# Optimization experiments

Measured on AMD Instinct MI355X. Metric: run time of the kernel, lower is better.

## Reference

```python
import jax, jax.numpy as jnp
import numpy as np

NB, CODES, D = 4, 1024, 64          # n_codebooks, codes_per_book, embedding_dim
B, T, H, W = 4, 8, 32, 32
COST = 0.25                          # commitment_cost


def setup_inputs() -> dict:
    key = jax.random.key(0)
    k1, k2 = jax.random.split(key)
    z = jax.random.normal(k1, (B, NB * D, T, H, W), dtype=jnp.float32)
    embeddings = jax.random.normal(k2, (NB, CODES, D), dtype=jnp.float32)
    return {"z": z, "embeddings": embeddings}


def reference(z, embeddings):
    # (B,C,T,H,W) -> (B,T,H,W,C) -> (NB, N, D) with N = B*T*H*W
    zc = jnp.moveaxis(z, 1, -1)
    flat = zc.reshape(-1, NB, D).transpose(1, 0, 2)  # (NB, N, D)
    N = flat.shape[1]

    x2 = jnp.sum(flat * flat, axis=2, keepdims=True)                 # (NB,N,1)
    e2 = jnp.sum(embeddings * embeddings, axis=2)[:, None, :]        # (NB,1,C)
    dist = x2 - 2.0 * jnp.einsum('knd,kcd->knc', flat, embeddings) + e2
    idx = jnp.argmin(dist, axis=2)                                   # (NB, N)

    # per-book embedding gather, equivalent to torch.stack([emb[i][idx[i]]], dim=-2)
    q = jax.vmap(lambda i, e: e[i])(idx, embeddings)                 # (NB, N, D)
    quantized = q.transpose(1, 0, 2).reshape(B, T, H, W, NB * D)
    quantized = jnp.moveaxis(quantized, -1, 1)                       # (B,C,T,H,W)

    encodings = jnp.moveaxis(idx.reshape(NB, B, T, H, W), 0, -1)     # (B,T,H,W,NB)

    commitment_loss = COST * jnp.mean((z - jax.lax.stop_gradient(quantized)) ** 2)
    quantized_st = z + jax.lax.stop_gradient(quantized - z)          # straight-through

    # perplexity from code usage histogram (avoids materializing one-hot)
    counts = jax.vmap(lambda i: jnp.zeros(CODES, flat.dtype).at[i].add(1.0))(idx)
    avg_probs = counts / N
    perplexity = jnp.mean(jnp.exp(-jnp.sum(avg_probs * jnp.log(avg_probs + 1e-10), axis=1)))

    return quantized_st, encodings, commitment_loss, perplexity
```

## Files before the change

kernel.cpp:

```cpp
#include <hip/hip_runtime.h>

#define NBOOKS 4
#define CODES  1024
#define DIM    64
#define NPOS   32768
#define CCH    256
#define ENC_OFF  8388608
#define LOSS_OFF 8519680
#define PERP_OFF 8519681

#define WS_E2      0
#define WS_EHI     16384
#define WS_ELO     540672
#define WS_IDX     1064960
#define WS_CNT     1589248
#define WS_PART    1605632
#define WS_FLAGCNT 1607680
#define WS_FLAGS   1607696

typedef _Float16 f16x8 __attribute__((ext_vector_type(8)));
typedef _Float16 f16x4 __attribute__((ext_vector_type(4)));
typedef float    f32x4 __attribute__((ext_vector_type(4)));

__global__ void k_eprep2(const float* __restrict__ emb, float* __restrict__ e2,
                         _Float16* __restrict__ ehi, _Float16* __restrict__ elo,
                         int* __restrict__ counts, int* __restrict__ flagcnt) {
    int i = blockIdx.x * 256 + threadIdx.x;
    counts[i] = 0;
    if (i == 0) *flagcnt = 0;
    const float4* e = (const float4*)(emb + ((size_t)i << 6));
    _Float16* hp = ehi + ((size_t)i << 6);
    _Float16* lp = elo + ((size_t)i << 6);
    float s = 0.f;
#pragma unroll
    for (int j = 0; j < 16; ++j) {
        float4 v = e[j];
        s += v.x * v.x + v.y * v.y + v.z * v.z + v.w * v.w;
        f16x4 hv, lv;
        float m;
        m = -2.f * v.x; hv[0] = (_Float16)m; lv[0] = (_Float16)(m - (float)hv[0]);
        m = -2.f * v.y; hv[1] = (_Float16)m; lv[1] = (_Float16)(m - (float)hv[1]);
        m = -2.f * v.z; hv[2] = (_Float16)m; lv[2] = (_Float16)(m - (float)hv[2]);
        m = -2.f * v.w; hv[3] = (_Float16)m; lv[3] = (_Float16)(m - (float)hv[3]);
        *(f16x4*)&hp[j * 4] = hv;
        *(f16x4*)&lp[j * 4] = lv;
    }
    e2[i] = s;
}

__global__ void __launch_bounds__(256, 4) k_argmin_mfma(
        const float* __restrict__ z, const float* __restrict__ e2g,
        const _Float16* __restrict__ ehi, const _Float16* __restrict__ elo,
        int* __restrict__ idxbuf, int* __restrict__ flagcnt,
        int* __restrict__ flaglist) {
    __shared__ __attribute__((aligned(16))) char sE[3][8192];

    int tid = threadIdx.x;
    int wave = tid >> 6, lane = tid & 63;
    int lrow = lane >> 4, lcol = lane & 15;
    int k = blockIdx.y;
    int posbase = blockIdx.x * 128;
    int b = posbase >> 13, s0 = posbase & 8191;
    int wb = wave * 32;

    const float* zb = z + (((size_t)(b * CCH + k * DIM)) << 13) + s0 + wb;
    f16x8 Xh[2][2], Xl[2][2];
#pragma unroll
    for (int pt = 0; pt < 2; ++pt)
#pragma unroll
        for (int kc = 0; kc < 2; ++kc) {
            f16x8 hv, lv;
#pragma unroll
            for (int e = 0; e < 8; ++e) {
                int d = kc * 32 + lrow * 8 + e;
                float f = zb[((size_t)d << 13) + pt * 16 + lcol];
                _Float16 h = (_Float16)f;
                hv[e] = h;
                lv[e] = (_Float16)(f - (float)h);
            }
            Xh[pt][kc] = hv; Xl[pt][kc] = lv;
        }

    int half = tid >> 7;
    int u = tid & 127;
    int r = u >> 2, q = u & 3;
    const char* bookh = (const char*)((half ? elo : ehi) + ((size_t)k << 16));
    const char* src0 = bookh + r * 128 + q * 32;
    int c0 = 2 * q, c1 = 2 * q + 1;
    int w0 = half * 4096 + r * 128 + ((c0 ^ (r & 7)) << 4);
    int w1 = half * 4096 + r * 128 + ((c1 ^ (r & 7)) << 4);

    const float* e2p = e2g + (k << 10) + lrow * 4;

    {
        f16x8 v0 = *(const f16x8*)(src0);
        f16x8 v1 = *(const f16x8*)(src0 + 16);
        *(f16x8*)&sE[0][w0] = v0;
        *(f16x8*)&sE[0][w1] = v1;
    }
    f32x4 ce2a = *(const f32x4*)(e2p);
    f32x4 ce2b = *(const f32x4*)(e2p + 16);

    float m1f[2][4], m2f[2][4];
#pragma unroll
    for (int pt = 0; pt < 2; ++pt)
#pragma unroll
        for (int rr = 0; rr < 4; ++rr) { m1f[pt][rr] = 3.4e38f; m2f[pt][rr] = 3.4e38f; }

    int sx = (lcol & 7) << 4;
    int o0 = (lrow << 4) ^ sx;
    int o1 = ((4 + lrow) << 4) ^ sx;
    int rbase = lcol << 7;

    int cur = 0, nxt = 1, fre = 2;
    for (int it = 0; it < 32; ++it) {
        __syncthreads();
        const char* sc = sE[cur];

        const char* rb0 = sc + rbase;
        const char* rb1 = sc + 2048 + rbase;
        f16x8 eh0a = *(const f16x8*)(rb0 + o0);
        f16x8 eh1a = *(const f16x8*)(rb0 + o1);
        f16x8 el0a = *(const f16x8*)(rb0 + 4096 + o0);
        f16x8 el1a = *(const f16x8*)(rb0 + 4096 + o1);
        f16x8 eh0b = *(const f16x8*)(rb1 + o0);
        f16x8 eh1b = *(const f16x8*)(rb1 + o1);
        f16x8 el0b = *(const f16x8*)(rb1 + 4096 + o0);
        f16x8 el1b = *(const f16x8*)(rb1 + 4096 + o1);

        f16x8 nv0, nv1;
        f32x4 ne2a, ne2b;
        bool has = it < 31;
        if (has) {
            const char* sp = src0 + (size_t)(it + 1) * 4096;
            nv0 = *(const f16x8*)(sp);
            nv1 = *(const f16x8*)(sp + 16);
            ne2a = *(const f32x4*)(e2p + (it + 1) * 32);
            ne2b = *(const f32x4*)(e2p + (it + 1) * 32 + 16);
        }

#pragma unroll
        for (int st = 0; st < 2; ++st) {
            f16x8 eh0 = st ? eh0b : eh0a;
            f16x8 eh1 = st ? eh1b : eh1a;
            f16x8 el0 = st ? el0b : el0a;
            f16x8 el1 = st ? el1b : el1a;
            f32x4 e2v = st ? ce2b : ce2a;
            unsigned kit = (unsigned)(it * 2 + st);
#pragma unroll
            for (int pt = 0; pt < 2; ++pt) {
                f32x4 acc = e2v;
                acc = __builtin_amdgcn_mfma_f32_16x16x32_f16(eh0, Xh[pt][0], acc, 0, 0, 0);
                acc = __builtin_amdgcn_mfma_f32_16x16x32_f16(eh0, Xl[pt][0], acc, 0, 0, 0);
                acc = __builtin_amdgcn_mfma_f32_16x16x32_f16(el0, Xh[pt][0], acc, 0, 0, 0);
                acc = __builtin_amdgcn_mfma_f32_16x16x32_f16(eh1, Xh[pt][1], acc, 0, 0, 0);
                acc = __builtin_amdgcn_mfma_f32_16x16x32_f16(eh1, Xl[pt][1], acc, 0, 0, 0);
                acc = __builtin_amdgcn_mfma_f32_16x16x32_f16(el1, Xh[pt][1], acc, 0, 0, 0);
#pragma unroll
                for (int rr = 0; rr < 4; ++rr) {
                    float key = __uint_as_float(
                        (__float_as_uint(acc[rr]) & 0xFFFFFFC0u) | kit);
                    m2f[pt][rr] = __builtin_amdgcn_fmed3f(m1f[pt][rr], m2f[pt][rr], key);
                    m1f[pt][rr] = fminf(m1f[pt][rr], key);
                }
            }
        }

        if (has) {
            *(f16x8*)&sE[nxt][w0] = nv0;
            *(f16x8*)&sE[nxt][w1] = nv1;
            ce2a = ne2a; ce2b = ne2b;
        }
        int t = cur; cur = nxt; nxt = fre; fre = t;
    }

    float F1[2], F2[2]; int I1[2];
#pragma unroll
    for (int pt = 0; pt < 2; ++pt) {
        float f1 = 3.4e38f, f2 = 3.4e38f; int i1 = 0;
#pragma unroll
        for (int rr = 0; rr < 4; ++rr) {
            unsigned mb = __float_as_uint(m1f[pt][rr]);
            float f = __uint_as_float(mb & 0xFFFFFFC0u);
            int   c = (int)(mb & 63u) * 16 + lrow * 4 + rr;
            float g = __uint_as_float(__float_as_uint(m2f[pt][rr]) & 0xFFFFFFC0u);
            bool take = (f < f1) || (f == f1 && c < i1);
            float loser = take ? f1 : f;
            f2 = fminf(fminf(f2, g), loser);
            if (take) { f1 = f; i1 = c; }
        }
        F1[pt] = f1; F2[pt] = f2; I1[pt] = i1;
    }

#pragma unroll
    for (int off = 16; off < 64; off <<= 1) {
#pragma unroll
        for (int pt = 0; pt < 2; ++pt) {
            float om1 = __shfl_xor(F1[pt], off);
            float om2 = __shfl_xor(F2[pt], off);
            int   oi  = __shfl_xor(I1[pt], off);
            bool take = (om1 < F1[pt]) || (om1 == F1[pt] && oi < I1[pt]);
            float loser = take ? F1[pt] : om1;
            F2[pt] = fminf(fminf(F2[pt], om2), loser);
            if (take) { F1[pt] = om1; I1[pt] = oi; }
        }
    }

    if (lane < 16) {
#pragma unroll
        for (int pt = 0; pt < 2; ++pt) {
            int n = posbase + wb + pt * 16 + lane;
            idxbuf[(k << 15) + n] = I1[pt];
            float thr = fmaf(fabsf(F1[pt]), 3.2e-5f, 2.0e-3f);
            if (F2[pt] - F1[pt] < thr) {
                int slot = atomicAdd(flagcnt, 1);
                flaglist[slot] = (k << 15) + n;
            }
        }
    }
}

__global__ void __launch_bounds__(256) k_rescore(
        const float* __restrict__ z, const float* __restrict__ emb,
        const float* __restrict__ e2g, const int* __restrict__ flagcnt,
        const int* __restrict__ flaglist, int* __restrict__ idxbuf) {
    __shared__ __attribute__((aligned(16))) float xsh[64];
    __shared__ float wbest[4];
    __shared__ int   wbi[4];
    int tid = threadIdx.x;
    int wave = tid >> 6, lane = tid & 63;
    int nf = *flagcnt;
    for (int e = blockIdx.x; e < nf; e += gridDim.x) {
        int gp = flaglist[e];
        int kk = gp >> 15, n = gp & 32767;
        int bb = n >> 13, s = n & 8191;
        __syncthreads();
        if (tid < 64)
            xsh[tid] = z[(((size_t)(bb * CCH + kk * DIM + tid)) << 13) + s];
        __syncthreads();

        const f32x4* ek4 = (const f32x4*)(emb + ((size_t)kk << 16));
        const float* ee  = e2g + (kk << 10);
        const f32x4* xr4 = (const f32x4*)xsh;
        float best = 3.4e38f; int bi = 0;
#pragma unroll
        for (int cc = 0; cc < 4; ++cc) {
            int c = cc * 256 + tid;
            const f32x4* ev = ek4 + (size_t)c * 16;
            float a0 = 0.f, a1 = 0.f, a2 = 0.f, a3 = 0.f;
#pragma unroll
            for (int j = 0; j < 16; ++j) {
                f32x4 xv = xr4[j];
                f32x4 qv = ev[j];
                a0 = fmaf(xv[0], qv[0], a0); a1 = fmaf(xv[1], qv[1], a1);
                a2 = fmaf(xv[2], qv[2], a2); a3 = fmaf(xv[3], qv[3], a3);
            }
            float dist = fmaf(-2.f, (a0 + a1) + (a2 + a3), ee[c]);
            if (dist < best) { best = dist; bi = c; }
        }
#pragma unroll
        for (int off = 1; off < 64; off <<= 1) {
            float ob = __shfl_xor(best, off);
            int   oi = __shfl_xor(bi, off);
            if (ob < best || (ob == best && oi < bi)) { best = ob; bi = oi; }
        }
        if (lane == 0) { wbest[wave] = best; wbi[wave] = bi; }
        __syncthreads();
        if (tid == 0) {
            float b0 = wbest[0]; int i0 = wbi[0];
#pragma unroll
            for (int w = 1; w < 4; ++w) {
                float bw = wbest[w]; int iw = wbi[w];
                if (bw < b0 || (bw == b0 && iw < i0)) { b0 = bw; i0 = iw; }
            }
            idxbuf[gp] = i0;
        }
    }
}

__global__ void __launch_bounds__(256) k_quant(
        const float* __restrict__ z, const float* __restrict__ emb,
        const int* __restrict__ idxbuf, float* __restrict__ out,
        int* __restrict__ counts, float* __restrict__ partial) {
    int tid = threadIdx.x;
    int q = blockIdx.x * 256 + tid;
    int n0 = q * 4;
    int k = blockIdx.y;
    int b = n0 >> 13;
    int s = n0 & 8191;

    int4 bi = *(const int4*)&idxbuf[(k << 15) + n0];
    const f32x4* e0 = (const f32x4*)(emb + ((size_t)k << 16) + ((size_t)bi.x << 6));
    const f32x4* e1 = (const f32x4*)(emb + ((size_t)k << 16) + ((size_t)bi.y << 6));
    const f32x4* e2 = (const f32x4*)(emb + ((size_t)k << 16) + ((size_t)bi.z << 6));
    const f32x4* e3 = (const f32x4*)(emb + ((size_t)k << 16) + ((size_t)bi.w << 6));
    size_t base = (((size_t)(b * CCH + k * DIM)) << 13) + s;

    float sq = 0.f;
#pragma unroll
    for (int j = 0; j < 16; ++j) {
        f32x4 q0 = e0[j], q1 = e1[j], q2 = e2[j], q3 = e3[j];
#pragma unroll
        for (int i = 0; i < 4; ++i) {
            int d = j * 4 + i;
            f32x4 zv = *(const f32x4*)(z + base + ((size_t)d << 13));
            f32x4 ov = {q0[i], q1[i], q2[i], q3[i]};
            *(f32x4*)(out + base + ((size_t)d << 13)) = ov;
            f32x4 df = zv - ov;
            sq = fmaf(df[0], df[0], sq);
            sq = fmaf(df[1], df[1], sq);
            sq = fmaf(df[2], df[2], sq);
            sq = fmaf(df[3], df[3], sq);
        }
    }

    out[ENC_OFF + (size_t)(n0 + 0) * NBOOKS + k] = (float)bi.x;
    out[ENC_OFF + (size_t)(n0 + 1) * NBOOKS + k] = (float)bi.y;
    out[ENC_OFF + (size_t)(n0 + 2) * NBOOKS + k] = (float)bi.z;
    out[ENC_OFF + (size_t)(n0 + 3) * NBOOKS + k] = (float)bi.w;
    atomicAdd(&counts[(k << 10) + bi.x], 1);
    atomicAdd(&counts[(k << 10) + bi.y], 1);
    atomicAdd(&counts[(k << 10) + bi.z], 1);
    atomicAdd(&counts[(k << 10) + bi.w], 1);

    for (int off = 32; off; off >>= 1) sq += __shfl_down(sq, off, 64);
    __shared__ float red[4];
    if ((tid & 63) == 0) red[tid >> 6] = sq;
    __syncthreads();
    if (tid == 0)
        partial[blockIdx.y * gridDim.x + blockIdx.x] = (red[0] + red[1]) + (red[2] + red[3]);
}

__global__ void __launch_bounds__(256) k_fin(
        const int* __restrict__ counts, const float* __restrict__ partial,
        float* __restrict__ out) {
    __shared__ float shl[4];
    __shared__ float shp[4];
    int tid = threadIdx.x;
    int wave = tid >> 6, lane = tid & 63;

    float s = tid < 128 ? partial[tid] : 0.f;
    for (int off = 32; off; off >>= 1) s += __shfl_down(s, off, 64);
    if (lane == 0) shl[wave] = s;

    float h = 0.f;
    const int* ck = counts + (wave << 10) + lane * 16;
#pragma unroll
    for (int j = 0; j < 16; ++j) {
        float p = (float)ck[j] * (1.f / 32768.f);
        h += p * logf(p + 1e-10f);
    }
    for (int off = 32; off; off >>= 1) h += __shfl_down(h, off, 64);
    if (lane == 0) shp[wave] = expf(-h);
    __syncthreads();
    if (tid == 0) {
        out[LOSS_OFF] = 0.25f * ((shl[0] + shl[1]) + (shl[2] + shl[3])) / 8388608.f;
        out[PERP_OFF] = 0.25f * ((shp[0] + shp[1]) + (shp[2] + shp[3]));
    }
}

extern "C" void kernel_launch(void* const* d_in, const int* in_sizes, int n_in,
                              void* d_out, int out_size, void* d_ws, size_t ws_size,
                              hipStream_t stream) {
    const float* z   = (const float*)d_in[0];
    const float* emb = (const float*)d_in[1];
    float* out = (float*)d_out;
    char* ws = (char*)d_ws;

    float*    e2       = (float*)(ws + WS_E2);
    _Float16* ehi      = (_Float16*)(ws + WS_EHI);
    _Float16* elo      = (_Float16*)(ws + WS_ELO);
    int*      idxbuf   = (int*)(ws + WS_IDX);
    int*      counts   = (int*)(ws + WS_CNT);
    float*    partial  = (float*)(ws + WS_PART);
    int*      flagcnt  = (int*)(ws + WS_FLAGCNT);
    int*      flaglist = (int*)(ws + WS_FLAGS);

    k_eprep2<<<16, 256, 0, stream>>>(emb, e2, ehi, elo, counts, flagcnt);

    dim3 agrid(NPOS / 128, NBOOKS);
    k_argmin_mfma<<<agrid, 256, 0, stream>>>(z, e2, ehi, elo, idxbuf, flagcnt, flaglist);
    k_rescore<<<1024, 256, 0, stream>>>(z, emb, e2, flagcnt, flaglist, idxbuf);

    dim3 qgrid(NPOS / 1024, NBOOKS);
    k_quant<<<qgrid, 256, 0, stream>>>(z, emb, idxbuf, out, counts, partial);
    k_fin<<<1, 256, 0, stream>>>(counts, partial, out);
}
```

Baseline: 113.9 us.

## Split codebook across waves and drop LDS staging in argmin kernel

Instead of each wave taking 32 positions and streaming all 1024 codes through triple-buffered shared memory, each wave now keeps all 128 positions of the block in registers and scans its own 256-code slice, loading codebook fragments straight from global memory with register prefetch. Per-wave results go through shared memory in a cross-wave reduction that keeps best and second-best distances. This removes the per-iteration barriers and LDS traffic, and each codebook fragment is reused across 8 position tiles. In exchange register use grows a lot (occupancy hint drops from 4 to 2), there is more global/L2 traffic for the codebook, and the near-tie threshold for flagging rescoring is tightened, which changes how many points get rescored.

```diff
diff --git a/kernel.cpp b/kernel.cpp
--- a/kernel.cpp
+++ b/kernel.cpp
@@ -48,12 +48,14 @@
     e2[i] = s;
 }
 
-__global__ void __launch_bounds__(256, 4) k_argmin_mfma(
+__global__ void __launch_bounds__(256, 2) k_argmin_mfma(
         const float* __restrict__ z, const float* __restrict__ e2g,
         const _Float16* __restrict__ ehi, const _Float16* __restrict__ elo,
         int* __restrict__ idxbuf, int* __restrict__ flagcnt,
         int* __restrict__ flaglist) {
-    __shared__ __attribute__((aligned(16))) char sE[3][8192];
+    __shared__ float sF1[512];
+    __shared__ float sF2[512];
+    __shared__ int   sI1[512];
 
     int tid = threadIdx.x;
     int wave = tid >> 6, lane = tid & 63;
@@ -61,161 +63,133 @@
     int k = blockIdx.y;
     int posbase = blockIdx.x * 128;
     int b = posbase >> 13, s0 = posbase & 8191;
-    int wb = wave * 32;
-
-    const float* zb = z + (((size_t)(b * CCH + k * DIM)) << 13) + s0 + wb;
-    f16x8 Xh[2][2], Xl[2][2];
-#pragma unroll
-    for (int pt = 0; pt < 2; ++pt)
+
+    const float* zb = z + (((size_t)(b * CCH + k * DIM)) << 13) + s0;
+    f16x8 Xh[8][2], Xl[8][2];
+#pragma unroll
+    for (int bt = 0; bt < 8; ++bt)
 #pragma unroll
         for (int kc = 0; kc < 2; ++kc) {
             f16x8 hv, lv;
 #pragma unroll
             for (int e = 0; e < 8; ++e) {
                 int d = kc * 32 + lrow * 8 + e;
-                float f = zb[((size_t)d << 13) + pt * 16 + lcol];
+                float f = zb[((size_t)d << 13) + bt * 16 + lcol];
                 _Float16 h = (_Float16)f;
                 hv[e] = h;
                 lv[e] = (_Float16)(f - (float)h);
             }
-            Xh[pt][kc] = hv; Xl[pt][kc] = lv;
-        }
-
-    int half = tid >> 7;
-    int u = tid & 127;
-    int r = u >> 2, q = u & 3;
-    const char* bookh = (const char*)((half ? elo : ehi) + ((size_t)k << 16));
-    const char* src0 = bookh + r * 128 + q * 32;
-    int c0 = 2 * q, c1 = 2 * q + 1;
-    int w0 = half * 4096 + r * 128 + ((c0 ^ (r & 7)) << 4);
-    int w1 = half * 4096 + r * 128 + ((c1 ^ (r & 7)) << 4);
-
-    const float* e2p = e2g + (k << 10) + lrow * 4;
-
-    {
-        f16x8 v0 = *(const f16x8*)(src0);
-        f16x8 v1 = *(const f16x8*)(src0 + 16);
-        *(f16x8*)&sE[0][w0] = v0;
-        *(f16x8*)&sE[0][w1] = v1;
-    }
-    f32x4 ce2a = *(const f32x4*)(e2p);
-    f32x4 ce2b = *(const f32x4*)(e2p + 16);
-
-    float m1f[2][4], m2f[2][4];
-#pragma unroll
-    for (int pt = 0; pt < 2; ++pt)
-#pragma unroll
-        for (int rr = 0; rr < 4; ++rr) { m1f[pt][rr] = 3.4e38f; m2f[pt][rr] = 3.4e38f; }
-
-    int sx = (lcol & 7) << 4;
-    int o0 = (lrow << 4) ^ sx;
-    int o1 = ((4 + lrow) << 4) ^ sx;
-    int rbase = lcol << 7;
-
-    int cur = 0, nxt = 1, fre = 2;
-    for (int it = 0; it < 32; ++it) {
-        __syncthreads();
-        const char* sc = sE[cur];
-
-        const char* rb0 = sc + rbase;
-        const char* rb1 = sc + 2048 + rbase;
-        f16x8 eh0a = *(const f16x8*)(rb0 + o0);
-        f16x8 eh1a = *(const f16x8*)(rb0 + o1);
-        f16x8 el0a = *(const f16x8*)(rb0 + 4096 + o0);
-        f16x8 el1a = *(const f16x8*)(rb0 + 4096 + o1);
-        f16x8 eh0b = *(const f16x8*)(rb1 + o0);
-        f16x8 eh1b = *(const f16x8*)(rb1 + o1);
-        f16x8 el0b = *(const f16x8*)(rb1 + 4096 + o0);
-        f16x8 el1b = *(const f16x8*)(rb1 + 4096 + o1);
-
-        f16x8 nv0, nv1;
-        f32x4 ne2a, ne2b;
-        bool has = it < 31;
+            Xh[bt][kc] = hv; Xl[bt][kc] = lv;
+        }
+
+    int slice = wave << 8;
+    const _Float16* ehp = ehi + ((size_t)k << 16) + (size_t)(slice + lcol) * 64 + lrow * 8;
+    const _Float16* elp = elo + ((size_t)k << 16) + (size_t)(slice + lcol) * 64 + lrow * 8;
+    const float*    e2p = e2g + (k << 10) + slice + lrow * 4;
+
+    f16x8 ceh0 = *(const f16x8*)(ehp);
+    f16x8 ceh1 = *(const f16x8*)(ehp + 32);
+    f16x8 cel0 = *(const f16x8*)(elp);
+    f16x8 cel1 = *(const f16x8*)(elp + 32);
+    f32x4 ce2  = *(const f32x4*)(e2p);
+
+    float m1[8][4], m2[8];
+#pragma unroll
+    for (int bt = 0; bt < 8; ++bt) {
+        m2[bt] = 3.4e38f;
+#pragma unroll
+        for (int rr = 0; rr < 4; ++rr) m1[bt][rr] = 3.4e38f;
+    }
+
+    for (int at = 0; at < 16; ++at) {
+        f16x8 neh0, neh1, nel0, nel1;
+        f32x4 ne2;
+        bool has = at < 15;
         if (has) {
-            const char* sp = src0 + (size_t)(it + 1) * 4096;
-            nv0 = *(const f16x8*)(sp);
-            nv1 = *(const f16x8*)(sp + 16);
-            ne2a = *(const f32x4*)(e2p + (it + 1) * 32);
-            ne2b = *(const f32x4*)(e2p + (it + 1) * 32 + 16);
-        }
-
-#pragma unroll
-        for (int st = 0; st < 2; ++st) {
-            f16x8 eh0 = st ? eh0b : eh0a;
-            f16x8 eh1 = st ? eh1b : eh1a;
-            f16x8 el0 = st ? el0b : el0a;
-            f16x8 el1 = st ? el1b : el1a;
-            f32x4 e2v = st ? ce2b : ce2a;
-            unsigned kit = (unsigned)(it * 2 + st);
-#pragma unroll
-            for (int pt = 0; pt < 2; ++pt) {
-                f32x4 acc = e2v;
-                acc = __builtin_amdgcn_mfma_f32_16x16x32_f16(eh0, Xh[pt][0], acc, 0, 0, 0);
-                acc = __builtin_amdgcn_mfma_f32_16x16x32_f16(eh0, Xl[pt][0], acc, 0, 0, 0);
-                acc = __builtin_amdgcn_mfma_f32_16x16x32_f16(el0, Xh[pt][0], acc, 0, 0, 0);
-                acc = __builtin_amdgcn_mfma_f32_16x16x32_f16(eh1, Xh[pt][1], acc, 0, 0, 0);
-                acc = __builtin_amdgcn_mfma_f32_16x16x32_f16(eh1, Xl[pt][1], acc, 0, 0, 0);
-                acc = __builtin_amdgcn_mfma_f32_16x16x32_f16(el1, Xh[pt][1], acc, 0, 0, 0);
-#pragma unroll
-                for (int rr = 0; rr < 4; ++rr) {
-                    float key = __uint_as_float(
-                        (__float_as_uint(acc[rr]) & 0xFFFFFFC0u) | kit);
-                    m2f[pt][rr] = __builtin_amdgcn_fmed3f(m1f[pt][rr], m2f[pt][rr], key);
-                    m1f[pt][rr] = fminf(m1f[pt][rr], key);
-                }
+            const _Float16* nh = ehp + (at + 1) * 1024;
+            const _Float16* nl = elp + (at + 1) * 1024;
+            neh0 = *(const f16x8*)(nh);
+            neh1 = *(const f16x8*)(nh + 32);
+            nel0 = *(const f16x8*)(nl);
+            nel1 = *(const f16x8*)(nl + 32);
+            ne2  = *(const f32x4*)(e2p + (at + 1) * 16);
+        }
+
+        unsigned kbase = (unsigned)(at * 4);
+#pragma unroll
+        for (int bt = 0; bt < 8; ++bt) {
+            f32x4 acc = ce2;
+            acc = __builtin_amdgcn_mfma_f32_16x16x32_f16(ceh0, Xh[bt][0], acc, 0, 0, 0);
+            acc = __builtin_amdgcn_mfma_f32_16x16x32_f16(ceh0, Xl[bt][0], acc, 0, 0, 0);
+            acc = __builtin_amdgcn_mfma_f32_16x16x32_f16(cel0, Xh[bt][0], acc, 0, 0, 0);
+            acc = __builtin_amdgcn_mfma_f32_16x16x32_f16(ceh1, Xh[bt][1], acc, 0, 0, 0);
+            acc = __builtin_amdgcn_mfma_f32_16x16x32_f16(ceh1, Xl[bt][1], acc, 0, 0, 0);
+            acc = __builtin_amdgcn_mfma_f32_16x16x32_f16(cel1, Xh[bt][1], acc, 0, 0, 0);
+#pragma unroll
+            for (int rr = 0; rr < 4; ++rr) {
+                float key = __uint_as_float(
+                    (__float_as_uint(acc[rr]) & 0xFFFFFFC0u) | (kbase + (unsigned)rr));
+                m2[bt]     = __builtin_amdgcn_fmed3f(m1[bt][rr], m2[bt], key);
+                m1[bt][rr] = fminf(m1[bt][rr], key);
             }
         }
-
         if (has) {
-            *(f16x8*)&sE[nxt][w0] = nv0;
-            *(f16x8*)&sE[nxt][w1] = nv1;
-            ce2a = ne2a; ce2b = ne2b;
-        }
-        int t = cur; cur = nxt; nxt = fre; fre = t;
-    }
-
-    float F1[2], F2[2]; int I1[2];
-#pragma unroll
-    for (int pt = 0; pt < 2; ++pt) {
-        float f1 = 3.4e38f, f2 = 3.4e38f; int i1 = 0;
-#pragma unroll
-        for (int rr = 0; rr < 4; ++rr) {
-            unsigned mb = __float_as_uint(m1f[pt][rr]);
-            float f = __uint_as_float(mb & 0xFFFFFFC0u);
-            int   c = (int)(mb & 63u) * 16 + lrow * 4 + rr;
-            float g = __uint_as_float(__float_as_uint(m2f[pt][rr]) & 0xFFFFFFC0u);
-            bool take = (f < f1) || (f == f1 && c < i1);
-            float loser = take ? f1 : f;
-            f2 = fminf(fminf(f2, g), loser);
-            if (take) { f1 = f; i1 = c; }
-        }
-        F1[pt] = f1; F2[pt] = f2; I1[pt] = i1;
-    }
-
-#pragma unroll
-    for (int off = 16; off < 64; off <<= 1) {
-#pragma unroll
-        for (int pt = 0; pt < 2; ++pt) {
-            float om1 = __shfl_xor(F1[pt], off);
-            float om2 = __shfl_xor(F2[pt], off);
-            int   oi  = __shfl_xor(I1[pt], off);
-            bool take = (om1 < F1[pt]) || (om1 == F1[pt] && oi < I1[pt]);
-            float loser = take ? F1[pt] : om1;
-            F2[pt] = fminf(fminf(F2[pt], om2), loser);
-            if (take) { F1[pt] = om1; I1[pt] = oi; }
-        }
-    }
-
-    if (lane < 16) {
-#pragma unroll
-        for (int pt = 0; pt < 2; ++pt) {
-            int n = posbase + wb + pt * 16 + lane;
-            idxbuf[(k << 15) + n] = I1[pt];
-            float thr = fmaf(fabsf(F1[pt]), 3.2e-5f, 2.0e-3f);
-            if (F2[pt] - F1[pt] < thr) {
-                int slot = atomicAdd(flagcnt, 1);
-                flaglist[slot] = (k << 15) + n;
-            }
+            ceh0 = neh0; ceh1 = neh1; cel0 = nel0; cel1 = nel1; ce2 = ne2;
+        }
+    }
+
+#pragma unroll
+    for (int bt = 0; bt < 8; ++bt) {
+        float a = m1[bt][0], bb2 = m1[bt][1], c = m1[bt][2], d = m1[bt][3];
+        float min01 = fminf(a, bb2), min23 = fminf(c, d);
+        float max01 = fmaxf(a, bb2), max23 = fmaxf(c, d);
+        float f1 = fminf(min01, min23);
+        float s2q = fminf(fmaxf(min01, min23), fminf(max01, max23));
+        float f2 = fminf(m2[bt], s2q);
+
+        unsigned mb = __float_as_uint(f1);
+        unsigned lm = mb & 63u;
+        int I1 = slice + (int)(lm >> 2) * 16 + lrow * 4 + (int)(lm & 3u);
+        float F1 = __uint_as_float(mb & 0xFFFFFFC0u);
+        float F2 = __uint_as_float(__float_as_uint(f2) & 0xFFFFFFC0u);
+
+#pragma unroll
+        for (int off = 16; off < 64; off <<= 1) {
+            float om1 = __shfl_xor(F1, off);
+            float om2 = __shfl_xor(F2, off);
+            int   oi  = __shfl_xor(I1, off);
+            bool take = (om1 < F1) || (om1 == F1 && oi < I1);
+            float loser = take ? F1 : om1;
+            F2 = fminf(fminf(F2, om2), loser);
+            if (take) { F1 = om1; I1 = oi; }
+        }
+        if (lane < 16) {
+            int p = bt * 16 + lane;
+            sF1[wave * 128 + p] = F1;
+            sF2[wave * 128 + p] = F2;
+            sI1[wave * 128 + p] = I1;
+        }
+    }
+    __syncthreads();
+
+    if (tid < 128) {
+        float a1 = sF1[tid], a2 = sF2[tid];
+        int   ai = sI1[tid];
+#pragma unroll
+        for (int w = 1; w < 4; ++w) {
+            float b1 = sF1[w * 128 + tid], b2 = sF2[w * 128 + tid];
+            int   bi = sI1[w * 128 + tid];
+            bool take = (b1 < a1) || (b1 == a1 && bi < ai);
+            float loser = take ? a1 : b1;
+            a2 = fminf(fminf(a2, b2), loser);
+            if (take) { a1 = b1; ai = bi; }
+        }
+        int n = posbase + tid;
+        idxbuf[(k << 15) + n] = ai;
+        float thr = fmaf(fabsf(a1), 1.6e-5f, 1.2e-3f);
+        if (a2 - a1 < thr) {
+            int slot = atomicAdd(flagcnt, 1);
+            flaglist[slot] = (k << 15) + n;
         }
     }
 }
```

New measurement: 113.1 us. About the same (-0.7%).

## Use single fp16 MFMA pass for argmin and widen rescore margin

Applied to the files above, without the earlier changes.

Drops the hi/lo fp16 split of embeddings and inputs, so the coarse argmin uses one fp16 MFMA product per K-chunk instead of three. This also halves the shared-memory tile and the global embedding traffic. To keep exact results, the ambiguity threshold that flags positions for fp32 rescoring is widened a lot. The trade is that more positions go to the rescore kernel, whose cost depends on how many are flagged.

```diff
diff --git a/kernel.cpp b/kernel.cpp
--- a/kernel.cpp
+++ b/kernel.cpp
@@ -11,7 +11,6 @@
 
 #define WS_E2      0
 #define WS_EHI     16384
-#define WS_ELO     540672
 #define WS_IDX     1064960
 #define WS_CNT     1589248
 #define WS_PART    1605632
@@ -23,37 +22,34 @@
 typedef float    f32x4 __attribute__((ext_vector_type(4)));
 
 __global__ void k_eprep2(const float* __restrict__ emb, float* __restrict__ e2,
-                         _Float16* __restrict__ ehi, _Float16* __restrict__ elo,
+                         _Float16* __restrict__ ehi,
                          int* __restrict__ counts, int* __restrict__ flagcnt) {
     int i = blockIdx.x * 256 + threadIdx.x;
     counts[i] = 0;
     if (i == 0) *flagcnt = 0;
     const float4* e = (const float4*)(emb + ((size_t)i << 6));
     _Float16* hp = ehi + ((size_t)i << 6);
-    _Float16* lp = elo + ((size_t)i << 6);
     float s = 0.f;
 #pragma unroll
     for (int j = 0; j < 16; ++j) {
         float4 v = e[j];
         s += v.x * v.x + v.y * v.y + v.z * v.z + v.w * v.w;
-        f16x4 hv, lv;
-        float m;
-        m = -2.f * v.x; hv[0] = (_Float16)m; lv[0] = (_Float16)(m - (float)hv[0]);
-        m = -2.f * v.y; hv[1] = (_Float16)m; lv[1] = (_Float16)(m - (float)hv[1]);
-        m = -2.f * v.z; hv[2] = (_Float16)m; lv[2] = (_Float16)(m - (float)hv[2]);
-        m = -2.f * v.w; hv[3] = (_Float16)m; lv[3] = (_Float16)(m - (float)hv[3]);
+        f16x4 hv;
+        hv[0] = (_Float16)(-2.f * v.x);
+        hv[1] = (_Float16)(-2.f * v.y);
+        hv[2] = (_Float16)(-2.f * v.z);
+        hv[3] = (_Float16)(-2.f * v.w);
         *(f16x4*)&hp[j * 4] = hv;
-        *(f16x4*)&lp[j * 4] = lv;
     }
     e2[i] = s;
 }
 
 __global__ void __launch_bounds__(256, 4) k_argmin_mfma(
         const float* __restrict__ z, const float* __restrict__ e2g,
-        const _Float16* __restrict__ ehi, const _Float16* __restrict__ elo,
+        const _Float16* __restrict__ ehi,
         int* __restrict__ idxbuf, int* __restrict__ flagcnt,
         int* __restrict__ flaglist) {
-    __shared__ __attribute__((aligned(16))) char sE[3][8192];
+    __shared__ __attribute__((aligned(16))) char sE[3][4096];
 
     int tid = threadIdx.x;
     int wave = tid >> 6, lane = tid & 63;
@@ -64,40 +60,29 @@
     int wb = wave * 32;
 
     const float* zb = z + (((size_t)(b * CCH + k * DIM)) << 13) + s0 + wb;
-    f16x8 Xh[2][2], Xl[2][2];
+    f16x8 Xh[2][2];
 #pragma unroll
     for (int pt = 0; pt < 2; ++pt)
 #pragma unroll
         for (int kc = 0; kc < 2; ++kc) {
-            f16x8 hv, lv;
+            f16x8 hv;
 #pragma unroll
             for (int e = 0; e < 8; ++e) {
                 int d = kc * 32 + lrow * 8 + e;
-                float f = zb[((size_t)d << 13) + pt * 16 + lcol];
-                _Float16 h = (_Float16)f;
-                hv[e] = h;
-                lv[e] = (_Float16)(f - (float)h);
-            }
-            Xh[pt][kc] = hv; Xl[pt][kc] = lv;
-        }
-
-    int half = tid >> 7;
-    int u = tid & 127;
-    int r = u >> 2, q = u & 3;
-    const char* bookh = (const char*)((half ? elo : ehi) + ((size_t)k << 16));
-    const char* src0 = bookh + r * 128 + q * 32;
-    int c0 = 2 * q, c1 = 2 * q + 1;
-    int w0 = half * 4096 + r * 128 + ((c0 ^ (r & 7)) << 4);
-    int w1 = half * 4096 + r * 128 + ((c1 ^ (r & 7)) << 4);
+                hv[e] = (_Float16)zb[((size_t)d << 13) + pt * 16 + lcol];
+            }
+            Xh[pt][kc] = hv;
+        }
+
+    int r = tid >> 3;
+    int q = tid & 7;
+    const char* bookh = (const char*)(ehi + ((size_t)k << 16));
+    const char* src0 = bookh + r * 128 + q * 16;
+    int w0 = r * 128 + ((q ^ (r & 7)) << 4);
 
     const float* e2p = e2g + (k << 10) + lrow * 4;
 
-    {
-        f16x8 v0 = *(const f16x8*)(src0);
-        f16x8 v1 = *(const f16x8*)(src0 + 16);
-        *(f16x8*)&sE[0][w0] = v0;
-        *(f16x8*)&sE[0][w1] = v1;
-    }
+    *(f16x8*)&sE[0][w0] = *(const f16x8*)(src0);
     f32x4 ce2a = *(const f32x4*)(e2p);
     f32x4 ce2b = *(const f32x4*)(e2p + 16);
 
@@ -107,34 +92,27 @@
 #pragma unroll
         for (int rr = 0; rr < 4; ++rr) { m1f[pt][rr] = 3.4e38f; m2f[pt][rr] = 3.4e38f; }
 
-    int sx = (lcol & 7) << 4;
-    int o0 = (lrow << 4) ^ sx;
-    int o1 = ((4 + lrow) << 4) ^ sx;
-    int rbase = lcol << 7;
+    int sxk = (lcol & 7);
+    int o0 = ((lrow ^ sxk) << 4);
+    int o1 = (((4 + lrow) ^ sxk) << 4);
+    int row0 = lcol << 7;
+    int row1 = (16 + lcol) << 7;
 
     int cur = 0, nxt = 1, fre = 2;
     for (int it = 0; it < 32; ++it) {
         __syncthreads();
         const char* sc = sE[cur];
 
-        const char* rb0 = sc + rbase;
-        const char* rb1 = sc + 2048 + rbase;
-        f16x8 eh0a = *(const f16x8*)(rb0 + o0);
-        f16x8 eh1a = *(const f16x8*)(rb0 + o1);
-        f16x8 el0a = *(const f16x8*)(rb0 + 4096 + o0);
-        f16x8 el1a = *(const f16x8*)(rb0 + 4096 + o1);
-        f16x8 eh0b = *(const f16x8*)(rb1 + o0);
-        f16x8 eh1b = *(const f16x8*)(rb1 + o1);
-        f16x8 el0b = *(const f16x8*)(rb1 + 4096 + o0);
-        f16x8 el1b = *(const f16x8*)(rb1 + 4096 + o1);
-
-        f16x8 nv0, nv1;
+        f16x8 eh0a = *(const f16x8*)(sc + row0 + o0);
+        f16x8 eh1a = *(const f16x8*)(sc + row0 + o1);
+        f16x8 eh0b = *(const f16x8*)(sc + row1 + o0);
+        f16x8 eh1b = *(const f16x8*)(sc + row1 + o1);
+
+        f16x8 nv0;
         f32x4 ne2a, ne2b;
         bool has = it < 31;
         if (has) {
-            const char* sp = src0 + (size_t)(it + 1) * 4096;
-            nv0 = *(const f16x8*)(sp);
-            nv1 = *(const f16x8*)(sp + 16);
+            nv0 = *(const f16x8*)(src0 + (size_t)(it + 1) * 4096);
             ne2a = *(const f32x4*)(e2p + (it + 1) * 32);
             ne2b = *(const f32x4*)(e2p + (it + 1) * 32 + 16);
         }
@@ -143,19 +121,13 @@
         for (int st = 0; st < 2; ++st) {
             f16x8 eh0 = st ? eh0b : eh0a;
             f16x8 eh1 = st ? eh1b : eh1a;
-            f16x8 el0 = st ? el0b : el0a;
-            f16x8 el1 = st ? el1b : el1a;
             f32x4 e2v = st ? ce2b : ce2a;
             unsigned kit = (unsigned)(it * 2 + st);
 #pragma unroll
             for (int pt = 0; pt < 2; ++pt) {
                 f32x4 acc = e2v;
                 acc = __builtin_amdgcn_mfma_f32_16x16x32_f16(eh0, Xh[pt][0], acc, 0, 0, 0);
-                acc = __builtin_amdgcn_mfma_f32_16x16x32_f16(eh0, Xl[pt][0], acc, 0, 0, 0);
-                acc = __builtin_amdgcn_mfma_f32_16x16x32_f16(el0, Xh[pt][0], acc, 0, 0, 0);
                 acc = __builtin_amdgcn_mfma_f32_16x16x32_f16(eh1, Xh[pt][1], acc, 0, 0, 0);
-                acc = __builtin_amdgcn_mfma_f32_16x16x32_f16(eh1, Xl[pt][1], acc, 0, 0, 0);
-                acc = __builtin_amdgcn_mfma_f32_16x16x32_f16(el1, Xh[pt][1], acc, 0, 0, 0);
 #pragma unroll
                 for (int rr = 0; rr < 4; ++rr) {
                     float key = __uint_as_float(
@@ -168,7 +140,6 @@
 
         if (has) {
             *(f16x8*)&sE[nxt][w0] = nv0;
-            *(f16x8*)&sE[nxt][w1] = nv1;
             ce2a = ne2a; ce2b = ne2b;
         }
         int t = cur; cur = nxt; nxt = fre; fre = t;
@@ -211,7 +182,7 @@
         for (int pt = 0; pt < 2; ++pt) {
             int n = posbase + wb + pt * 16 + lane;
             idxbuf[(k << 15) + n] = I1[pt];
-            float thr = fmaf(fabsf(F1[pt]), 3.2e-5f, 2.0e-3f);
+            float thr = fmaf(fabsf(F1[pt]), 3.2e-5f, 5.0e-2f);
             if (F2[pt] - F1[pt] < thr) {
                 int slot = atomicAdd(flagcnt, 1);
                 flaglist[slot] = (k << 15) + n;
@@ -369,17 +340,16 @@
 
     float*    e2       = (float*)(ws + WS_E2);
     _Float16* ehi      = (_Float16*)(ws + WS_EHI);
-    _Float16* elo      = (_Float16*)(ws + WS_ELO);
     int*      idxbuf   = (int*)(ws + WS_IDX);
     int*      counts   = (int*)(ws + WS_CNT);
     float*    partial  = (float*)(ws + WS_PART);
     int*      flagcnt  = (int*)(ws + WS_FLAGCNT);
     int*      flaglist = (int*)(ws + WS_FLAGS);
 
-    k_eprep2<<<16, 256, 0, stream>>>(emb, e2, ehi, elo, counts, flagcnt);
+    k_eprep2<<<16, 256, 0, stream>>>(emb, e2, ehi, counts, flagcnt);
 
     dim3 agrid(NPOS / 128, NBOOKS);
-    k_argmin_mfma<<<agrid, 256, 0, stream>>>(z, e2, ehi, elo, idxbuf, flagcnt, flaglist);
+    k_argmin_mfma<<<agrid, 256, 0, stream>>>(z, e2, ehi, idxbuf, flagcnt, flaglist);
     k_rescore<<<1024, 256, 0, stream>>>(z, emb, e2, flagcnt, flaglist, idxbuf);
 
     dim3 qgrid(NPOS / 1024, NBOOKS);
```

Result: slower. 143.9 us (+26.3%).
